# Kernel optimization log

Measured on AMD Instinct MI355X. Metric: run time of the kernel, lower is better.

Reference implementation:

```python
import jax, jax.numpy as jnp
import numpy as np

DIL = 2      # dilation of deformable depthwise conv (padding == dilation -> same size)
EPS = 1e-5   # BatchNorm eps
B, C, O, G, H, W = 4, 256, 256, 64, 64, 64


def conv2d(x, w, padding, dilation=1):
    return jax.lax.conv_general_dilated(
        x, w, window_strides=(1, 1), padding=[(padding, padding)] * 2,
        rhs_dilation=(dilation, dilation),
        dimension_numbers=("NCHW", "OIHW", "NCHW"))


def bn_inf(x, gamma, beta, mean, var):
    scale = (gamma / jnp.sqrt(var + EPS))[None, :, None, None]
    return (x - mean[None, :, None, None]) * scale + beta[None, :, None, None]


def bilinear_gather(xt, ys, xs):
    # xt: [B,H,W,C]; ys, xs: [B,K,H,W] float sample coords. Zero padding outside.
    Bb, Hh, Ww, Cc = xt.shape
    y0 = jnp.floor(ys)
    x0 = jnp.floor(xs)
    wy = (ys - y0)[..., None]
    wx = (xs - x0)[..., None]
    bidx = jnp.arange(Bb)[:, None, None, None]

    def gather(yi, xi):
        valid = (yi >= 0) & (yi < Hh) & (xi >= 0) & (xi < Ww)
        yc = jnp.clip(yi, 0, Hh - 1).astype(jnp.int32)
        xc = jnp.clip(xi, 0, Ww - 1).astype(jnp.int32)
        val = xt[bidx, yc, xc]            # [B,K,H,W,C]
        return val * valid[..., None].astype(xt.dtype)

    v00 = gather(y0, x0)
    v01 = gather(y0, x0 + 1)
    v10 = gather(y0 + 1, x0)
    v11 = gather(y0 + 1, x0 + 1)
    return (v00 * (1 - wy) * (1 - wx) + v01 * (1 - wy) * wx
            + v10 * wy * (1 - wx) + v11 * wy * wx)


def setup_inputs() -> dict:
    key = jax.random.key(0)
    ks = jax.random.split(key, 12)
    inp = {
        "x": jax.random.normal(ks[0], (B, C, H, W), jnp.float32),
        "grad_feats": jax.random.normal(ks[1], (B, G, H, W), jnp.float32),
        # offset block: conv3x3(G->18) + BN + ReLU
        "off_w": jax.random.normal(ks[2], (18, G, 3, 3), jnp.float32) / np.sqrt(G * 9),
        "off_gamma": 1.0 + 0.1 * jax.random.normal(ks[3], (18,), jnp.float32),
        "off_beta": 0.1 * jax.random.normal(ks[4], (18,), jnp.float32),
        "off_mean": 0.1 * jax.random.normal(ks[5], (18,), jnp.float32),
        "off_var": jax.random.uniform(ks[6], (18,), jnp.float32, 0.5, 1.5),
        # deformable separable conv: depthwise 3x3 (per-channel) then pointwise 1x1, no bias
        "dw_w": jax.random.normal(ks[7], (C, 3, 3), jnp.float32) / 3.0,
        "pw_w": jax.random.normal(ks[8], (O, C), jnp.float32) / np.sqrt(C),
        # output BN
        "bn_gamma": 1.0 + 0.1 * jax.random.normal(ks[9], (O,), jnp.float32),
        "bn_beta": 0.1 * jax.random.normal(ks[10], (O,), jnp.float32),
        "bn_mean": 0.1 * jax.random.normal(ks[11], (O,), jnp.float32),
        "bn_var": jnp.ones((O,), jnp.float32),
    }
    return inp


def reference(x, grad_feats, off_w, off_gamma, off_beta, off_mean, off_var,
              dw_w, pw_w, bn_gamma, bn_beta, bn_mean, bn_var):
    Bb, Cc, Hh, Ww = x.shape
    # offset block: conv3x3 + BN + ReLU -> [B,18,H,W]
    off = jax.nn.relu(bn_inf(conv2d(grad_feats, off_w, 1),
                             off_gamma, off_beta, off_mean, off_var))
    off = off.reshape(Bb, 9, 2, Hh, Ww)
    dy, dx = off[:, :, 0], off[:, :, 1]                     # [B,9,H,W]
    # base kernel grid: padding == dilation so tap offsets are (kh-1)*DIL
    kk = (jnp.arange(3, dtype=jnp.float32) - 1.0) * DIL
    ky = jnp.repeat(kk, 3)                                   # [9] row offsets
    kx = jnp.tile(kk, 3)                                     # [9] col offsets
    gy = jnp.arange(Hh, dtype=jnp.float32)[None, None, :, None] + ky[None, :, None, None] + dy
    gx = jnp.arange(Ww, dtype=jnp.float32)[None, None, None, :] + kx[None, :, None, None] + dx
    samp = bilinear_gather(x.transpose(0, 2, 3, 1), gy, gx)  # [B,9,H,W,C]
    out = jnp.einsum("bkhwc,ck->bchw", samp, dw_w.reshape(Cc, 9))   # depthwise
    out = jnp.einsum("bchw,oc->bohw", out, pw_w)                    # pointwise 1x1
    out = jax.nn.relu(bn_inf(out, bn_gamma, bn_beta, bn_mean, bn_var))
    return out
```

## Files before the change

kernel.cpp:

```cpp
#include <hip/hip_runtime.h>
#include <stdint.h>

#define Bn 4
#define Cn 256
#define On 256
#define Gn 64
#define Hn 64
#define Wn 64
#define HWn 4096
#define EPSf 1e-5f

#define WS_XT    0u
#define WS_OFF   8388608u
#define WS_PWB   9568256u

typedef __attribute__((ext_vector_type(8))) short short8;
typedef __attribute__((ext_vector_type(4))) float f4;

__device__ __forceinline__ unsigned int bfround(float f) {
    unsigned int u = __float_as_uint(f);
    u += 0x7FFFu + ((u >> 16) & 1u);
    return u >> 16;
}
__device__ __forceinline__ float blo(unsigned u) { return __uint_as_float(u << 16); }
__device__ __forceinline__ float bhi(unsigned u) { return __uint_as_float(u & 0xFFFF0000u); }

__global__ __launch_bounds__(256, 4) void k_pre(const float* __restrict__ x,
                                                const float* __restrict__ pw_w,
                                                char* __restrict__ ws)
{
    __shared__ float smem[4160];
    int tid = threadIdx.x, bid = blockIdx.x;

    if (bid < 1024) {
        unsigned short* xt = (unsigned short*)(ws + WS_XT);
        int pt = bid & 63, ct = (bid >> 6) & 3, b = bid >> 8;
        int p0 = pt * 64, c0 = ct * 64;
        const float4* x4 = (const float4*)(x + (size_t)b * Cn * HWn);
        #pragma unroll
        for (int it = 0; it < 4; ++it) {
            int v = it * 256 + tid;
            int ci = v >> 4, pj = v & 15;
            float4 f = x4[(size_t)(c0 + ci) * 1024 + (p0 >> 2) + pj];
            smem[ci * 65 + pj * 4 + 0] = f.x;
            smem[ci * 65 + pj * 4 + 1] = f.y;
            smem[ci * 65 + pj * 4 + 2] = f.z;
            smem[ci * 65 + pj * 4 + 3] = f.w;
        }
        __syncthreads();
        unsigned short* xtb = xt + (size_t)b * HWn * Cn;
        #pragma unroll
        for (int it = 0; it < 2; ++it) {
            int u = it * 256 + tid;
            int pi = u >> 3, cj = u & 7;
            float f[8];
            #pragma unroll
            for (int j = 0; j < 8; ++j)
                f[j] = smem[(cj * 8 + j) * 65 + pi];
            uint4 pk;
            pk.x = bfround(f[0]) | (bfround(f[1]) << 16);
            pk.y = bfround(f[2]) | (bfround(f[3]) << 16);
            pk.z = bfround(f[4]) | (bfround(f[5]) << 16);
            pk.w = bfround(f[6]) | (bfround(f[7]) << 16);
            *(uint4*)(xtb + (size_t)(p0 + pi) * Cn + c0 + cj * 8) = pk;
        }
        return;
    }
    unsigned short* pwb = (unsigned short*)(ws + WS_PWB);
    const float4* p4 = (const float4*)pw_w;
    uint2* o2 = (uint2*)pwb;
    int base = (bid - 1024) * 512;
    #pragma unroll
    for (int i = 0; i < 2; ++i) {
        int id2 = base + i * 256 + tid;
        float4 f = p4[id2];
        uint2 pk;
        pk.x = bfround(f.x) | (bfround(f.y) << 16);
        pk.y = bfround(f.z) | (bfround(f.w) << 16);
        o2[id2] = pk;
    }
}

__global__ __launch_bounds__(256, 4) void k_off(const float* __restrict__ gf,
                                                const float* __restrict__ off_w,
                                                const float* __restrict__ og,
                                                const float* __restrict__ obt,
                                                const float* __restrict__ om,
                                                const float* __restrict__ ov,
                                                char* __restrict__ ws)
{
    __shared__ float swt[10368];
    __shared__ float sred[4 * 18 * 65];
    float* __restrict__ off = (float*)(ws + WS_OFF);
    int tid = threadIdx.x;
    int h = blockIdx.x, b = blockIdx.y;
    int lane = tid & 63;
    int wvU = __builtin_amdgcn_readfirstlane(tid >> 6);

    for (int i = tid; i < 10368; i += 256) {
        int ch = i / 576;
        int rem = i - ch * 576;
        int g = rem / 9;
        int r9 = rem - g * 9;
        int ty = r9 / 3, tx = r9 - ty * 3;
        swt[(g * 3 + ty) * 54 + tx * 18 + ch] = off_w[i];
    }
    __syncthreads();

    float acc[18];
    #pragma unroll
    for (int ch = 0; ch < 18; ++ch) acc[ch] = 0.f;

    const float* gfb = gf + (size_t)b * Gn * HWn;
    for (int gi = 0; gi < 16; ++gi) {
        int g = wvU * 16 + gi;
        const float* gfg = gfb + (size_t)g * HWn;
        float rv[3], su[3], sd[3];
        #pragma unroll
        for (int r = 0; r < 3; ++r) {
            int y = h - 1 + r;
            rv[r] = ((unsigned)y < 64u) ? gfg[y * 64 + lane] : 0.f;
        }
        #pragma unroll
        for (int r = 0; r < 3; ++r) {
            float u = __shfl_up(rv[r], 1);   su[r] = (lane == 0)  ? 0.f : u;
            float d = __shfl_down(rv[r], 1); sd[r] = (lane == 63) ? 0.f : d;
        }
        #pragma unroll
        for (int ty = 0; ty < 3; ++ty) {
            const float* wrow = &swt[(g * 3 + ty) * 54];
            #pragma unroll
            for (int ch = 0; ch < 18; ++ch)
                acc[ch] += wrow[ch] * su[ty] + wrow[18 + ch] * rv[ty] + wrow[36 + ch] * sd[ty];
        }
    }

    #pragma unroll
    for (int ch = 0; ch < 18; ++ch)
        sred[(wvU * 18 + ch) * 65 + lane] = acc[ch];
    __syncthreads();

    float* obp = off + (size_t)(b * HWn + h * 64) * 18;
    for (int i = tid; i < 1152; i += 256) {
        int w = i / 18, ch = i - w * 18;
        float v = sred[ch * 65 + w] + sred[(18 + ch) * 65 + w]
                + sred[(36 + ch) * 65 + w] + sred[(54 + ch) * 65 + w];
        float s = og[ch] * rsqrtf(ov[ch] + EPSf);
        v = (v - om[ch]) * s + obt[ch];
        obp[i] = v > 0.f ? v : 0.f;
    }
}

#define TLD 264
__global__ __launch_bounds__(512, 4) void k_fuse(float* __restrict__ out,
                                                 const float* __restrict__ dw_w,
                                                 const float* __restrict__ bg,
                                                 const float* __restrict__ bb,
                                                 const float* __restrict__ bm,
                                                 const float* __restrict__ bv,
                                                 const char* __restrict__ ws)
{
    const unsigned short* __restrict__ xt  = (const unsigned short*)(ws + WS_XT);
    const unsigned short* __restrict__ pwb = (const unsigned short*)(ws + WS_PWB);
    const float* __restrict__ off = (const float*)(ws + WS_OFF);
    __shared__ float smeta[288 * 8];
    __shared__ float sdw[9 * 256];
    __shared__ unsigned short tl[32 * TLD];

    int bid = blockIdx.x;
    int xcd = bid & 7, slot = bid >> 3;
    int b = xcd >> 1;
    int h = ((xcd & 1) << 5) | (slot >> 1);
    int w0 = (slot & 1) << 5;
    int tid = threadIdx.x;

    for (int i = tid; i < 2304; i += 512) {
        int k = i >> 8, c = i & 255;
        sdw[i] = dw_w[c * 9 + k];
    }

    if (tid < 288) {
        int k = tid >> 5, wl = tid & 31;
        int w = w0 + wl;
        int kyi = k / 3, kxi = k - kyi * 3;
        const float* op = off + ((size_t)(b * HWn + h * 64 + w)) * 18 + 2 * k;
        float dy = op[0], dx = op[1];
        float gy = (float)(h + (kyi - 1) * 2) + dy;
        float gx = (float)(w + (kxi - 1) * 2) + dx;
        float fy = floorf(gy), fx = floorf(gx);
        float wy = gy - fy, wx = gx - fx;
        int y0 = (int)fy, x0 = (int)fx;
        int y1 = y0 + 1, x1 = x0 + 1;
        float m00 = ((unsigned)y0 < 64u && (unsigned)x0 < 64u) ? 1.f : 0.f;
        float m01 = ((unsigned)y0 < 64u && (unsigned)x1 < 64u) ? 1.f : 0.f;
        float m10 = ((unsigned)y1 < 64u && (unsigned)x0 < 64u) ? 1.f : 0.f;
        float m11 = ((unsigned)y1 < 64u && (unsigned)x1 < 64u) ? 1.f : 0.f;
        int y0c = min(max(y0, 0), 63), y1c = min(max(y1, 0), 63);
        int x0c = min(max(x0, 0), 63), x1c = min(max(x1, 0), 63);
        float4 mw;
        mw.x = (1.f - wy) * (1.f - wx) * m00;
        mw.y = (1.f - wy) * wx * m01;
        mw.z = wy * (1.f - wx) * m10;
        mw.w = wy * wx * m11;
        float4 mo;
        mo.x = __int_as_float((y0c * 64 + x0c) << 9);
        mo.y = __int_as_float((y0c * 64 + x1c) << 9);
        mo.z = __int_as_float((y1c * 64 + x0c) << 9);
        mo.w = __int_as_float((y1c * 64 + x1c) << 9);
        float4* s4w = (float4*)smeta;
        s4w[(k * 32 + wl) * 2] = mw;
        s4w[(k * 32 + wl) * 2 + 1] = mo;
    }
    __syncthreads();

    int lane = tid & 63, wave = tid >> 6;
    int half = lane >> 5, c8 = lane & 31;
    int c0 = c8 * 8;

    const char* xb = (const char*)(xt + (size_t)b * HWn * Cn);
    int laneByte = c8 * 16;
    const float4* s4 = (const float4*)smeta;
    #pragma unroll
    for (int iter = 0; iter < 2; ++iter) {
        int wl = iter * 16 + wave * 2 + half;
        float acc[8];
        #pragma unroll
        for (int j = 0; j < 8; ++j) acc[j] = 0.f;
        #pragma unroll
        for (int k = 0; k < 9; ++k) {
            float4 mw = s4[(k * 32 + wl) * 2];
            float4 mo = s4[(k * 32 + wl) * 2 + 1];
            float4 d0 = *(const float4*)(&sdw[k * 256 + c0]);
            float4 d1 = *(const float4*)(&sdw[k * 256 + c0 + 4]);
            uint4 qA = *(const uint4*)(xb + __float_as_int(mo.x) + laneByte);
            uint4 qB = *(const uint4*)(xb + __float_as_int(mo.y) + laneByte);
            uint4 qC = *(const uint4*)(xb + __float_as_int(mo.z) + laneByte);
            uint4 qD = *(const uint4*)(xb + __float_as_int(mo.w) + laneByte);
            const unsigned* uA = (const unsigned*)&qA;
            const unsigned* uB = (const unsigned*)&qB;
            const unsigned* uC = (const unsigned*)&qC;
            const unsigned* uD = (const unsigned*)&qD;
            const float* dk = (const float*)&d0;
            #pragma unroll
            for (int j = 0; j < 4; ++j) {
                const float* dkj = (j < 2) ? dk : (const float*)&d1;
                int jj = (j & 1) * 2;
                float sl = mw.x * blo(uA[j]) + mw.y * blo(uB[j]) + mw.z * blo(uC[j]) + mw.w * blo(uD[j]);
                float sh = mw.x * bhi(uA[j]) + mw.y * bhi(uB[j]) + mw.z * bhi(uC[j]) + mw.w * bhi(uD[j]);
                acc[2 * j]     += sl * dkj[jj];
                acc[2 * j + 1] += sh * dkj[jj + 1];
            }
        }
        uint4 pk;
        pk.x = bfround(acc[0]) | (bfround(acc[1]) << 16);
        pk.y = bfround(acc[2]) | (bfround(acc[3]) << 16);
        pk.z = bfround(acc[4]) | (bfround(acc[5]) << 16);
        pk.w = bfround(acc[6]) | (bfround(acc[7]) << 16);
        *(uint4*)(&tl[wl * TLD + c0]) = pk;
    }
    __syncthreads();

    int m0 = wave * 32;
    int row = lane & 15, quad = lane >> 4;
    f4 acc[2][2];
    #pragma unroll
    for (int i = 0; i < 2; ++i)
        #pragma unroll
        for (int j = 0; j < 2; ++j)
            acc[i][j] = (f4){0.f, 0.f, 0.f, 0.f};

    #pragma unroll 2
    for (int kq = 0; kq < 8; ++kq) {
        int kk = kq * 32 + quad * 8;
        short8 a[2], bf[2];
        #pragma unroll
        for (int mt = 0; mt < 2; ++mt)
            a[mt] = *(const short8*)(pwb + (size_t)(m0 + mt * 16 + row) * Cn + kk);
        #pragma unroll
        for (int nt = 0; nt < 2; ++nt)
            bf[nt] = *(const short8*)(&tl[(nt * 16 + row) * TLD + kk]);
        #pragma unroll
        for (int mt = 0; mt < 2; ++mt)
            #pragma unroll
            for (int nt = 0; nt < 2; ++nt)
                acc[mt][nt] = __builtin_amdgcn_mfma_f32_16x16x32_bf16(a[mt], bf[nt], acc[mt][nt], 0, 0, 0);
    }

    float* obp = out + (size_t)b * On * HWn + h * 64 + w0;
    #pragma unroll
    for (int mt = 0; mt < 2; ++mt) {
        #pragma unroll
        for (int r = 0; r < 4; ++r) {
            int o = m0 + mt * 16 + quad * 4 + r;
            float s = bg[o] * rsqrtf(bv[o] + EPSf);
            float sh = bb[o] - bm[o] * s;
            #pragma unroll
            for (int nt = 0; nt < 2; ++nt) {
                float v = acc[mt][nt][r] * s + sh;
                v = v > 0.f ? v : 0.f;
                obp[(size_t)o * HWn + nt * 16 + row] = v;
            }
        }
    }
}

extern "C" void kernel_launch(void* const* d_in, const int* in_sizes, int n_in,
                              void* d_out, int out_size, void* d_ws, size_t ws_size,
                              hipStream_t stream)
{
    const float* x     = (const float*)d_in[0];
    const float* gf    = (const float*)d_in[1];
    const float* off_w = (const float*)d_in[2];
    const float* og    = (const float*)d_in[3];
    const float* ob    = (const float*)d_in[4];
    const float* om    = (const float*)d_in[5];
    const float* ov    = (const float*)d_in[6];
    const float* dw_w  = (const float*)d_in[7];
    const float* pw_w  = (const float*)d_in[8];
    const float* bg    = (const float*)d_in[9];
    const float* bb    = (const float*)d_in[10];
    const float* bm    = (const float*)d_in[11];
    const float* bv    = (const float*)d_in[12];
    float* out = (float*)d_out;
    char* ws = (char*)d_ws;

    hipLaunchKernelGGL(k_pre, dim3(1056), dim3(256), 0, stream, x, pw_w, ws);
    hipLaunchKernelGGL(k_off, dim3(Hn, Bn), dim3(256), 0, stream,
                       gf, off_w, og, ob, om, ov, ws);
    hipLaunchKernelGGL(k_fuse, dim3(512), dim3(512), 0, stream,
                       out, dw_w, bg, bb, bm, bv, ws);
}
```

Baseline: 170.0 us.

## Pretranspose offset weights once, raise fuse occupancy, use nontemporal output stores

The offset-conv weight transpose moves out of every k_off block into one extra k_pre block, which writes the transposed weights to workspace. k_off then loads them with plain float4 copies instead of scattered, division-heavy index math. The change also unrolls k_off's channel loop by two, raises k_fuse launch bounds to 8 blocks, and writes the final output with nontemporal stores. Higher launch bounds may force register spills in k_fuse, and the extra k_pre block adds a small serial tail.

```diff
diff --git a/kernel.cpp b/kernel.cpp
--- a/kernel.cpp
+++ b/kernel.cpp
@@ -13,6 +13,7 @@
 #define WS_XT    0u
 #define WS_OFF   8388608u
 #define WS_PWB   9568256u
+#define WS_WT    9699328u
 
 typedef __attribute__((ext_vector_type(8))) short short8;
 typedef __attribute__((ext_vector_type(4))) float f4;
@@ -27,6 +28,7 @@
 
 __global__ __launch_bounds__(256, 4) void k_pre(const float* __restrict__ x,
                                                 const float* __restrict__ pw_w,
+                                                const float* __restrict__ off_w,
                                                 char* __restrict__ ws)
 {
     __shared__ float smem[4160];
@@ -66,23 +68,36 @@
         }
         return;
     }
-    unsigned short* pwb = (unsigned short*)(ws + WS_PWB);
-    const float4* p4 = (const float4*)pw_w;
-    uint2* o2 = (uint2*)pwb;
-    int base = (bid - 1024) * 512;
-    #pragma unroll
-    for (int i = 0; i < 2; ++i) {
-        int id2 = base + i * 256 + tid;
-        float4 f = p4[id2];
-        uint2 pk;
-        pk.x = bfround(f.x) | (bfround(f.y) << 16);
-        pk.y = bfround(f.z) | (bfround(f.w) << 16);
-        o2[id2] = pk;
+    if (bid < 1056) {
+        unsigned short* pwb = (unsigned short*)(ws + WS_PWB);
+        const float4* p4 = (const float4*)pw_w;
+        uint2* o2 = (uint2*)pwb;
+        int base = (bid - 1024) * 512;
+        #pragma unroll
+        for (int i = 0; i < 2; ++i) {
+            int id2 = base + i * 256 + tid;
+            float4 f = p4[id2];
+            uint2 pk;
+            pk.x = bfround(f.x) | (bfround(f.y) << 16);
+            pk.y = bfround(f.z) | (bfround(f.w) << 16);
+            o2[id2] = pk;
+        }
+        return;
+    }
+    {
+        float* wT = (float*)(ws + WS_WT);
+        for (int i = tid; i < 10368; i += 256) {
+            int ch = i / 576;
+            int rem = i - ch * 576;
+            int g = rem / 9;
+            int r9 = rem - g * 9;
+            int ty = r9 / 3, tx = r9 - ty * 3;
+            wT[(g * 3 + ty) * 54 + tx * 18 + ch] = off_w[i];
+        }
     }
 }
 
 __global__ __launch_bounds__(256, 4) void k_off(const float* __restrict__ gf,
-                                                const float* __restrict__ off_w,
                                                 const float* __restrict__ og,
                                                 const float* __restrict__ obt,
                                                 const float* __restrict__ om,
@@ -91,19 +106,21 @@
 {
     __shared__ float swt[10368];
     __shared__ float sred[4 * 18 * 65];
+    const float* __restrict__ wT = (const float*)(ws + WS_WT);
     float* __restrict__ off = (float*)(ws + WS_OFF);
     int tid = threadIdx.x;
     int h = blockIdx.x, b = blockIdx.y;
     int lane = tid & 63;
     int wvU = __builtin_amdgcn_readfirstlane(tid >> 6);
 
-    for (int i = tid; i < 10368; i += 256) {
-        int ch = i / 576;
-        int rem = i - ch * 576;
-        int g = rem / 9;
-        int r9 = rem - g * 9;
-        int ty = r9 / 3, tx = r9 - ty * 3;
-        swt[(g * 3 + ty) * 54 + tx * 18 + ch] = off_w[i];
+    {
+        const float4* w4 = (const float4*)wT;
+        float4* s4 = (float4*)swt;
+        #pragma unroll
+        for (int j = 0; j < 11; ++j) {
+            int idx = j * 256 + tid;
+            if (idx < 2592) s4[idx] = w4[idx];
+        }
     }
     __syncthreads();
 
@@ -112,6 +129,7 @@
     for (int ch = 0; ch < 18; ++ch) acc[ch] = 0.f;
 
     const float* gfb = gf + (size_t)b * Gn * HWn;
+    #pragma unroll 2
     for (int gi = 0; gi < 16; ++gi) {
         int g = wvU * 16 + gi;
         const float* gfg = gfb + (size_t)g * HWn;
@@ -152,7 +170,7 @@
 }
 
 #define TLD 264
-__global__ __launch_bounds__(512, 4) void k_fuse(float* __restrict__ out,
+__global__ __launch_bounds__(512, 8) void k_fuse(float* __restrict__ out,
                                                  const float* __restrict__ dw_w,
                                                  const float* __restrict__ bg,
                                                  const float* __restrict__ bb,
@@ -240,10 +258,11 @@
             const unsigned* uB = (const unsigned*)&qB;
             const unsigned* uC = (const unsigned*)&qC;
             const unsigned* uD = (const unsigned*)&qD;
-            const float* dk = (const float*)&d0;
+            const float* dk0 = (const float*)&d0;
+            const float* dk1 = (const float*)&d1;
             #pragma unroll
             for (int j = 0; j < 4; ++j) {
-                const float* dkj = (j < 2) ? dk : (const float*)&d1;
+                const float* dkj = (j < 2) ? dk0 : dk1;
                 int jj = (j & 1) * 2;
                 float sl = mw.x * blo(uA[j]) + mw.y * blo(uB[j]) + mw.z * blo(uC[j]) + mw.w * blo(uD[j]);
                 float sh = mw.x * bhi(uA[j]) + mw.y * bhi(uB[j]) + mw.z * bhi(uC[j]) + mw.w * bhi(uD[j]);
@@ -298,7 +317,7 @@
             for (int nt = 0; nt < 2; ++nt) {
                 float v = acc[mt][nt][r] * s + sh;
                 v = v > 0.f ? v : 0.f;
-                obp[(size_t)o * HWn + nt * 16 + row] = v;
+                __builtin_nontemporal_store(v, &obp[(size_t)o * HWn + nt * 16 + row]);
             }
         }
     }
@@ -324,9 +343,9 @@
     float* out = (float*)d_out;
     char* ws = (char*)d_ws;
 
-    hipLaunchKernelGGL(k_pre, dim3(1056), dim3(256), 0, stream, x, pw_w, ws);
+    hipLaunchKernelGGL(k_pre, dim3(1057), dim3(256), 0, stream, x, pw_w, off_w, ws);
     hipLaunchKernelGGL(k_off, dim3(Hn, Bn), dim3(256), 0, stream,
-                       gf, off_w, og, ob, om, ov, ws);
+                       gf, og, ob, om, ov, ws);
     hipLaunchKernelGGL(k_fuse, dim3(512), dim3(512), 0, stream,
                        out, dw_w, bg, bb, bm, bv, ws);
 }
```

After: 256.5 us. 50.9% more time.
